# Performance work log

Measured on AMD Instinct MI355X. Metric: run time of the kernel, lower is better.

## Reference

```python
import jax, jax.numpy as jnp
import numpy as np
from jax import lax

SKIP = 0.3      # graph_skip_conn
STEPS = 5       # GGNN propagation steps
HEADS = 16
T, B, N, D = 16, 32, 256, 128
NUM_CLASSES = 2
EPS = 1e-8


def setup_inputs() -> dict:
    key = jax.random.key(0)
    ks = jax.random.split(key, 12)
    s = 0.05
    return {
        "inputs": jax.random.normal(ks[0], (T, B, N, D), dtype=jnp.float32),
        "supports": jax.random.uniform(ks[1], (B, N, N), dtype=jnp.float32),
        # multi-head weighted-cosine graph learner weights
        "W_gl": jax.random.normal(ks[2], (HEADS, D), dtype=jnp.float32) * s,
        # GGNN message transform
        "W_a": jax.random.normal(ks[3], (D, D), dtype=jnp.float32) * s,
        "b_a": jnp.zeros((D,), dtype=jnp.float32),
        # GGNN gated propagator (GRU-style) over concat([a, h]) -> D
        "W_r": jax.random.normal(ks[4], (2 * D, D), dtype=jnp.float32) * s,
        "b_r": jnp.zeros((D,), dtype=jnp.float32),
        "W_z": jax.random.normal(ks[5], (2 * D, D), dtype=jnp.float32) * s,
        "b_z": jnp.zeros((D,), dtype=jnp.float32),
        "W_h": jax.random.normal(ks[6], (2 * D, D), dtype=jnp.float32) * s,
        "b_h": jnp.zeros((D,), dtype=jnp.float32),
        # final classifier
        "W_fc": jax.random.normal(ks[7], (N * D, NUM_CLASSES), dtype=jnp.float32) * s,
        "b_fc": jnp.zeros((NUM_CLASSES,), dtype=jnp.float32),
    }


def _cell(x, A, W_gl, W_a, b_a, W_r, b_r, W_z, b_z, W_h, b_h):
    # ---- graph learner: multi-head weighted cosine similarity ----
    # x: (B,N,D); W_gl: (H,D)
    xw = x[None, :, :, :] * W_gl[:, None, None, :]             # (H,B,N,D)
    xw = xw / (jnp.linalg.norm(xw, axis=-1, keepdims=True) + EPS)
    att = jnp.einsum("hbnd,hbmd->hbnm", xw, xw).mean(axis=0)   # (B,N,N)
    att = jax.nn.relu(att)
    att = att / (att.sum(axis=-1, keepdims=True) + EPS)        # row-normalize
    A_new = SKIP * A + (1.0 - SKIP) * att                      # skip connection

    # ---- GGNN propagation over learned adjacency ----
    h = x
    for _ in range(STEPS):
        a = jnp.einsum("bnm,bmd->bnd", A_new, h) @ W_a + b_a   # message
        ah = jnp.concatenate([a, h], axis=-1)                  # (B,N,2D)
        r = jax.nn.sigmoid(ah @ W_r + b_r)
        z = jax.nn.sigmoid(ah @ W_z + b_z)
        h_tilde = jnp.tanh(jnp.concatenate([a, r * h], axis=-1) @ W_h + b_h)
        h = (1.0 - z) * h + z * h_tilde
    return h, A_new


def reference(inputs, supports, W_gl, W_a, b_a, W_r, b_r, W_z, b_z, W_h, b_h, W_fc, b_fc):
    def step(A, x_t):
        h, A_new = _cell(x_t, A, W_gl, W_a, b_a, W_r, b_r, W_z, b_z, W_h, b_h)
        return A_new, h

    A_final, outs = lax.scan(step, supports, inputs)           # outs: (T,B,N,D)
    last = outs[-1]                                            # (B,N,D)
    logits = last.reshape(last.shape[0], -1) @ W_fc + b_fc     # (B,C)
    return logits
```

## Files before the change

kernel.cpp:

```cpp
#include <hip/hip_runtime.h>
#include <math.h>

#define TT 16
#define BB 32
#define NN 256
#define DD 128
#define NSTEPS 5
#define SKIPF 0.3f
#define EPSF 1e-8f
#define T0 7
#define TBLIVE ((TT - T0) * BB)
#define IVSTR 257


typedef __attribute__((ext_vector_type(8))) short bf16x8;
typedef __attribute__((ext_vector_type(4))) float f32x4;
typedef __attribute__((ext_vector_type(8))) _Float16 half8;
typedef __attribute__((ext_vector_type(2))) _Float16 h2;

__device__ __forceinline__ unsigned short f2bf(float f) {
    union { float f; unsigned u; } v; v.f = f;
    unsigned r = (v.u + 0x7FFF + ((v.u >> 16) & 1)) >> 16;
    return (unsigned short)r;
}
__device__ __forceinline__ float bf2f(unsigned short u) {
    union { unsigned u; float f; } v; v.u = ((unsigned)u) << 16; return v.f;
}
__device__ __forceinline__ unsigned pack2(unsigned short a, unsigned short b) {
    return (unsigned)a | ((unsigned)b << 16);
}
__device__ __forceinline__ unsigned pkrtz(float a, float b) {
    unsigned r;
    asm("v_cvt_pkrtz_f16_f32 %0, %1, %2" : "=v"(r) : "v"(a), "v"(b));
    return r;
}
__device__ __forceinline__ h2 u2h(unsigned u) {
    union { unsigned u; h2 h; } v; v.u = u; return v.h;
}
__device__ __forceinline__ float sigmoidf_(float x) {
    return 1.0f / (1.0f + __expf(-x));
}
__device__ __forceinline__ float tanhf_(float x) {
    return 1.0f - 2.0f / (__expf(2.0f * x) + 1.0f);
}
__device__ __forceinline__ half8 ld8f32h(const float* src) {
    float4 a = *(const float4*)src;
    float4 b = *(const float4*)(src + 4);
    uint4 o;
    o.x = pkrtz(a.x, a.y); o.y = pkrtz(a.z, a.w);
    o.z = pkrtz(b.x, b.y); o.w = pkrtz(b.z, b.w);
    union { uint4 u; half8 h; } v; v.u = o; return v.h;
}

__global__ __launch_bounds__(256, 2) void k_gram2(const float* __restrict__ x,
                                                  const float* __restrict__ Wgl,
                                                  unsigned short* __restrict__ attn) {
    int bid = blockIdx.x;
    int rg = bid / TBLIVE;
    int tb = T0 * BB + (bid - rg * TBLIVE);
    int n0 = rg << 6;
    int tid = threadIdx.x;
    int wave = tid >> 6, lane = tid & 63;
    int m16 = lane & 15, quad = lane >> 4;
    int wcol = wave << 6;

    __shared__ unsigned wS[16 * 64];
    __shared__ unsigned ivS[16 * IVSTR];
    __shared__ float rsum[4][64];

    const float* Xb = x + ((size_t)tb << 15);

    #pragma unroll
    for (int k = 0; k < 4; ++k) {
        int idx = (tid << 2) + k;
        float2 wv = *(const float2*)(Wgl + ((idx >> 6) << 7) + ((idx & 63) << 1));
        wS[idx] = pkrtz(wv.x * wv.x, wv.y * wv.y);
    }

    half8 Bf[4][4];
    #pragma unroll
    for (int ks = 0; ks < 4; ++ks)
        #pragma unroll
        for (int cb = 0; cb < 4; ++cb)
            Bf[ks][cb] = ld8f32h(Xb + ((wcol + (cb << 4) + m16) << 7) + (ks << 5) + (quad << 3));

    half8 Af[4][4];
    #pragma unroll
    for (int rb = 0; rb < 4; ++rb)
        #pragma unroll
        for (int ks = 0; ks < 4; ++ks)
            Af[rb][ks] = ld8f32h(Xb + ((n0 + (rb << 4) + m16) << 7) + (ks << 5) + (quad << 3));

    f32x4 att[4][4];
    #pragma unroll
    for (int rb = 0; rb < 4; ++rb)
        #pragma unroll
        for (int cb = 0; cb < 4; ++cb) att[rb][cb] = (f32x4){0.f, 0.f, 0.f, 0.f};

    __syncthreads();

    union H8 { half8 v; h2 p[4]; };

    {
        half8 w2f[4];
        #pragma unroll
        for (int ks = 0; ks < 4; ++ks)
            w2f[ks] = *(const half8*)((const unsigned short*)wS + (m16 << 7) + (ks << 5) + (quad << 3));
        #pragma unroll
        for (int cb = 0; cb < 4; ++cb) {
            f32x4 nacc = (f32x4){0.f, 0.f, 0.f, 0.f};
            #pragma unroll
            for (int ks = 0; ks < 4; ++ks) {
                H8 bb; bb.v = Bf[ks][cb];
                H8 sq;
                sq.p[0] = bb.p[0] * bb.p[0];
                sq.p[1] = bb.p[1] * bb.p[1];
                sq.p[2] = bb.p[2] * bb.p[2];
                sq.p[3] = bb.p[3] * bb.p[3];
                nacc = __builtin_amdgcn_mfma_f32_16x16x32_f16(sq.v, w2f[ks], nacc, 0, 0, 0);
            }
            #pragma unroll
            for (int r = 0; r < 4; ++r) {
                float inv = 1.0f / (sqrtf(nacc[r]) + EPSF);
                ivS[m16 * IVSTR + wcol + (cb << 4) + (quad << 2) + r] = pkrtz(inv, inv);
            }
        }
    }
    __syncthreads();

    #pragma unroll 1
    for (int h = 0; h < 16; ++h) {
        const unsigned* ivh = ivS + h * IVSTR;
        h2 ivr[4], ivc[4];
        #pragma unroll
        for (int rb = 0; rb < 4; ++rb) ivr[rb] = u2h(ivh[n0 + (rb << 4) + m16]);
        #pragma unroll
        for (int cb = 0; cb < 4; ++cb) ivc[cb] = u2h(ivh[wcol + (cb << 4) + m16]);

        #pragma unroll
        for (int ks = 0; ks < 4; ++ks) {
            uint4 wu = *(const uint4*)(wS + (h << 6) + (ks << 4) + (quad << 2));
            h2 w0 = u2h(wu.x), w1 = u2h(wu.y), w2 = u2h(wu.z), w3 = u2h(wu.w);

            H8 afr[4];
            #pragma unroll
            for (int rb = 0; rb < 4; ++rb) {
                H8 a; a.v = Af[rb][ks];
                h2 s = ivr[rb];
                afr[rb].p[0] = a.p[0] * (w0 * s);
                afr[rb].p[1] = a.p[1] * (w1 * s);
                afr[rb].p[2] = a.p[2] * (w2 * s);
                afr[rb].p[3] = a.p[3] * (w3 * s);
            }
            #pragma unroll
            for (int cb = 0; cb < 4; ++cb) {
                H8 b; b.v = Bf[ks][cb];
                H8 bf;
                bf.p[0] = b.p[0] * ivc[cb];
                bf.p[1] = b.p[1] * ivc[cb];
                bf.p[2] = b.p[2] * ivc[cb];
                bf.p[3] = b.p[3] * ivc[cb];
                #pragma unroll
                for (int rb = 0; rb < 4; ++rb)
                    att[rb][cb] = __builtin_amdgcn_mfma_f32_16x16x32_f16(afr[rb].v, bf.v, att[rb][cb], 0, 0, 0);
            }
        }
    }

    float rs[4][4];
    #pragma unroll
    for (int rb = 0; rb < 4; ++rb)
        #pragma unroll
        for (int r = 0; r < 4; ++r) {
            float s = 0.f;
            #pragma unroll
            for (int cb = 0; cb < 4; ++cb) {
                float v = fmaxf(att[rb][cb][r], 0.0f);
                att[rb][cb][r] = v;
                s += v;
            }
            rs[rb][r] = s;
        }
    #pragma unroll
    for (int m = 1; m < 16; m <<= 1)
        #pragma unroll
        for (int rb = 0; rb < 4; ++rb)
            #pragma unroll
            for (int r = 0; r < 4; ++r)
                rs[rb][r] += __shfl_xor(rs[rb][r], m, 64);
    if (m16 == 0) {
        #pragma unroll
        for (int rb = 0; rb < 4; ++rb)
            #pragma unroll
            for (int r = 0; r < 4; ++r)
                rsum[wave][(rb << 4) + (quad << 2) + r] = rs[rb][r];
    }
    __syncthreads();

    unsigned short* outb = attn + ((size_t)tb << 16);
    #pragma unroll
    for (int rb = 0; rb < 4; ++rb) {
        #pragma unroll
        for (int r = 0; r < 4; ++r) {
            int row = (rb << 4) + (quad << 2) + r;
            float tot = rsum[0][row] + rsum[1][row] + rsum[2][row] + rsum[3][row];
            float inv = (1.0f - SKIPF) / (tot + 16.0f * EPSF);
            #pragma unroll
            for (int cb = 0; cb < 4; ++cb) {
                int col = wcol + (cb << 4) + m16;
                outb[((size_t)(n0 + row) << 8) + col] = f2bf(att[rb][cb][r] * inv);
            }
        }
    }
}

__global__ __launch_bounds__(256) void k_scanh(const float* __restrict__ supports,
                                               const unsigned short* __restrict__ AttA,
                                               const float* __restrict__ x15,
                                               const float* __restrict__ Wa,
                                               const float* __restrict__ Wr,
                                               const float* __restrict__ Wz,
                                               const float* __restrict__ Wh,
                                               unsigned short* __restrict__ Afin,
                                               unsigned short* __restrict__ hT,
                                               unsigned short* __restrict__ WaT,
                                               unsigned short* __restrict__ WrT,
                                               unsigned short* __restrict__ WzT,
                                               unsigned short* __restrict__ WhT) {
    __shared__ float tl[32][33];
    int bid = blockIdx.x;
    int tid = threadIdx.x;
    if (bid < 2048) {
        size_t flat = ((size_t)bid * 256 + tid) * 4;
        float4 s4 = *(const float4*)(supports + flat);
        const float s7 = SKIPF * SKIPF * SKIPF * SKIPF * SKIPF * SKIPF * SKIPF;
        float a0 = s4.x * s7, a1 = s4.y * s7, a2 = s4.z * s7, a3 = s4.w * s7;
        #pragma unroll
        for (int t = T0; t < TT; ++t) {
            const unsigned short* p = AttA + ((size_t)t << 21) + flat;
            uint2 u = *(const uint2*)p;
            a0 = SKIPF * a0 + bf2f((unsigned short)(u.x & 0xffff));
            a1 = SKIPF * a1 + bf2f((unsigned short)(u.x >> 16));
            a2 = SKIPF * a2 + bf2f((unsigned short)(u.y & 0xffff));
            a3 = SKIPF * a3 + bf2f((unsigned short)(u.y >> 16));
        }
        uint2 o;
        o.x = pack2(f2bf(a0), f2bf(a1));
        o.y = pack2(f2bf(a2), f2bf(a3));
        *(uint2*)(Afin + flat) = o;
    } else if (bid < 3072) {
        int b2 = bid - 2048;
        int b = b2 >> 5; int r = b2 & 31; int d0 = (r >> 3) << 5; int n0 = (r & 7) << 5;
        int i = tid >> 5, j = tid & 31;
        #pragma unroll
        for (int s = 0; s < 4; ++s) {
            int nl = (s << 3) + i;
            tl[nl][j] = x15[((size_t)(b * 256 + n0 + nl) << 7) + d0 + j];
        }
        __syncthreads();
        #pragma unroll
        for (int s = 0; s < 4; ++s) {
            int dd = (s << 3) + i;
            hT[((size_t)(b * 128 + d0 + dd) << 8) + n0 + j] = f2bf(tl[j][dd]);
        }
    } else {
        int idx = (bid - 3072) * 256 + tid;
        if (idx < 16384) {
            int dout = idx >> 7, din = idx & 127;
            WaT[idx] = f2bf(Wa[(din << 7) + dout]);
        }
        {
            int dout = idx >> 8, dk = idx & 255;
            WrT[idx] = f2bf(Wr[(dk << 7) + dout]);
            WzT[idx] = f2bf(Wz[(dk << 7) + dout]);
            WhT[idx] = f2bf(Wh[(dk << 7) + dout]);
        }
    }
}

__global__ __launch_bounds__(256) void k_step(
    const unsigned short* __restrict__ Afin,
    const unsigned short* __restrict__ hT,
    const unsigned short* __restrict__ WaT, const float* __restrict__ ba,
    const unsigned short* __restrict__ WrT, const float* __restrict__ br,
    const unsigned short* __restrict__ WzT, const float* __restrict__ bz,
    const unsigned short* __restrict__ WhT, const float* __restrict__ bh,
    unsigned short* __restrict__ hT_o) {

    int bid = blockIdx.x;
    int b = bid & 31, rg = bid >> 5;
    int n0 = rg << 5;
    int tid = threadIdx.x;
    int wave = tid >> 6, lane = tid & 63;
    int m16 = lane & 15, quad = lane >> 4;
    int wcol = wave << 5;

    __shared__ unsigned short msgS[32 * 136];
    __shared__ unsigned short ahS[32 * 264];

    const unsigned short* hTb = hT + ((size_t)b << 15);

    #pragma unroll
    for (int j = 0; j < 16; ++j) {
        int idx = (j << 8) + tid;
        int d = idx >> 5, row = idx & 31;
        ahS[row * 264 + 128 + d] = hTb[((size_t)d << 8) + n0 + row];
    }

    f32x4 acc[2][2];
    #pragma unroll
    for (int rb = 0; rb < 2; ++rb)
        #pragma unroll
        for (int cb = 0; cb < 2; ++cb) acc[rb][cb] = (f32x4){0.f, 0.f, 0.f, 0.f};

    const unsigned short* Ab = Afin + ((size_t)b << 16) + ((size_t)n0 << 8);
    #pragma unroll 2
    for (int ks = 0; ks < 8; ++ks) {
        bf16x8 af[2], bf[2];
        #pragma unroll
        for (int rb = 0; rb < 2; ++rb)
            af[rb] = *(const bf16x8*)(Ab + (((rb << 4) + m16) << 8) + (ks << 5) + (quad << 3));
        #pragma unroll
        for (int cb = 0; cb < 2; ++cb)
            bf[cb] = *(const bf16x8*)(hTb + ((wcol + (cb << 4) + m16) << 8) + (ks << 5) + (quad << 3));
        #pragma unroll
        for (int rb = 0; rb < 2; ++rb)
            #pragma unroll
            for (int cb = 0; cb < 2; ++cb)
                acc[rb][cb] = __builtin_amdgcn_mfma_f32_16x16x32_bf16(af[rb], bf[cb], acc[rb][cb], 0, 0, 0);
    }
    #pragma unroll
    for (int rb = 0; rb < 2; ++rb)
        #pragma unroll
        for (int cb = 0; cb < 2; ++cb)
            #pragma unroll
            for (int r = 0; r < 4; ++r)
                msgS[((rb << 4) + (quad << 2) + r) * 136 + wcol + (cb << 4) + m16] = f2bf(acc[rb][cb][r]);
    __syncthreads();

    #pragma unroll
    for (int rb = 0; rb < 2; ++rb)
        #pragma unroll
        for (int cb = 0; cb < 2; ++cb) acc[rb][cb] = (f32x4){0.f, 0.f, 0.f, 0.f};
    #pragma unroll
    for (int ks = 0; ks < 4; ++ks) {
        bf16x8 af[2], bf[2];
        #pragma unroll
        for (int rb = 0; rb < 2; ++rb)
            af[rb] = *(const bf16x8*)(msgS + ((rb << 4) + m16) * 136 + (ks << 5) + (quad << 3));
        #pragma unroll
        for (int cb = 0; cb < 2; ++cb)
            bf[cb] = *(const bf16x8*)(WaT + ((wcol + (cb << 4) + m16) << 7) + (ks << 5) + (quad << 3));
        #pragma unroll
        for (int rb = 0; rb < 2; ++rb)
            #pragma unroll
            for (int cb = 0; cb < 2; ++cb)
                acc[rb][cb] = __builtin_amdgcn_mfma_f32_16x16x32_bf16(af[rb], bf[cb], acc[rb][cb], 0, 0, 0);
    }
    {
        float bav[2];
        #pragma unroll
        for (int cb = 0; cb < 2; ++cb) bav[cb] = ba[wcol + (cb << 4) + m16];
        #pragma unroll
        for (int rb = 0; rb < 2; ++rb)
            #pragma unroll
            for (int cb = 0; cb < 2; ++cb)
                #pragma unroll
                for (int r = 0; r < 4; ++r)
                    ahS[((rb << 4) + (quad << 2) + r) * 264 + wcol + (cb << 4) + m16] =
                        f2bf(acc[rb][cb][r] + bav[cb]);
    }
    __syncthreads();

    float hv[2][2][4];
    #pragma unroll
    for (int rb = 0; rb < 2; ++rb)
        #pragma unroll
        for (int cb = 0; cb < 2; ++cb) {
            int col = wcol + (cb << 4) + m16;
            uint2 u = *(const uint2*)(hTb + ((size_t)col << 8) + n0 + (rb << 4) + (quad << 2));
            hv[rb][cb][0] = bf2f((unsigned short)(u.x & 0xffff));
            hv[rb][cb][1] = bf2f((unsigned short)(u.x >> 16));
            hv[rb][cb][2] = bf2f((unsigned short)(u.y & 0xffff));
            hv[rb][cb][3] = bf2f((unsigned short)(u.y >> 16));
        }

    f32x4 racc[2][2], zacc[2][2];
    #pragma unroll
    for (int rb = 0; rb < 2; ++rb)
        #pragma unroll
        for (int cb = 0; cb < 2; ++cb) {
            racc[rb][cb] = (f32x4){0.f, 0.f, 0.f, 0.f};
            zacc[rb][cb] = (f32x4){0.f, 0.f, 0.f, 0.f};
        }
    #pragma unroll 2
    for (int ks = 0; ks < 8; ++ks) {
        bf16x8 af[2], bfr[2], bfz[2];
        #pragma unroll
        for (int rb = 0; rb < 2; ++rb)
            af[rb] = *(const bf16x8*)(ahS + ((rb << 4) + m16) * 264 + (ks << 5) + (quad << 3));
        #pragma unroll
        for (int cb = 0; cb < 2; ++cb) {
            int dout = wcol + (cb << 4) + m16;
            bfr[cb] = *(const bf16x8*)(WrT + (dout << 8) + (ks << 5) + (quad << 3));
            bfz[cb] = *(const bf16x8*)(WzT + (dout << 8) + (ks << 5) + (quad << 3));
        }
        #pragma unroll
        for (int rb = 0; rb < 2; ++rb)
            #pragma unroll
            for (int cb = 0; cb < 2; ++cb) {
                racc[rb][cb] = __builtin_amdgcn_mfma_f32_16x16x32_bf16(af[rb], bfr[cb], racc[rb][cb], 0, 0, 0);
                zacc[rb][cb] = __builtin_amdgcn_mfma_f32_16x16x32_bf16(af[rb], bfz[cb], zacc[rb][cb], 0, 0, 0);
            }
    }
    float zv[2][2][4];
    {
        float brv[2], bzv[2];
        #pragma unroll
        for (int cb = 0; cb < 2; ++cb) {
            brv[cb] = br[wcol + (cb << 4) + m16];
            bzv[cb] = bz[wcol + (cb << 4) + m16];
        }
        #pragma unroll
        for (int rb = 0; rb < 2; ++rb)
            #pragma unroll
            for (int cb = 0; cb < 2; ++cb)
                #pragma unroll
                for (int r = 0; r < 4; ++r) {
                    racc[rb][cb][r] = sigmoidf_(racc[rb][cb][r] + brv[cb]);
                    zv[rb][cb][r]  = sigmoidf_(zacc[rb][cb][r] + bzv[cb]);
                }
    }
    __syncthreads();

    #pragma unroll
    for (int rb = 0; rb < 2; ++rb)
        #pragma unroll
        for (int cb = 0; cb < 2; ++cb)
            #pragma unroll
            for (int r = 0; r < 4; ++r)
                ahS[((rb << 4) + (quad << 2) + r) * 264 + 128 + wcol + (cb << 4) + m16] =
                    f2bf(racc[rb][cb][r] * hv[rb][cb][r]);
    __syncthreads();

    #pragma unroll
    for (int rb = 0; rb < 2; ++rb)
        #pragma unroll
        for (int cb = 0; cb < 2; ++cb) acc[rb][cb] = (f32x4){0.f, 0.f, 0.f, 0.f};
    #pragma unroll 2
    for (int ks = 0; ks < 8; ++ks) {
        bf16x8 af[2], bf[2];
        #pragma unroll
        for (int rb = 0; rb < 2; ++rb)
            af[rb] = *(const bf16x8*)(ahS + ((rb << 4) + m16) * 264 + (ks << 5) + (quad << 3));
        #pragma unroll
        for (int cb = 0; cb < 2; ++cb)
            bf[cb] = *(const bf16x8*)(WhT + ((wcol + (cb << 4) + m16) << 8) + (ks << 5) + (quad << 3));
        #pragma unroll
        for (int rb = 0; rb < 2; ++rb)
            #pragma unroll
            for (int cb = 0; cb < 2; ++cb)
                acc[rb][cb] = __builtin_amdgcn_mfma_f32_16x16x32_bf16(af[rb], bf[cb], acc[rb][cb], 0, 0, 0);
    }

    {
        float bhv[2];
        #pragma unroll
        for (int cb = 0; cb < 2; ++cb) bhv[cb] = bh[wcol + (cb << 4) + m16];
        #pragma unroll
        for (int rb = 0; rb < 2; ++rb)
            #pragma unroll
            for (int cb = 0; cb < 2; ++cb) {
                int col = wcol + (cb << 4) + m16;
                unsigned short pk[4];
                #pragma unroll
                for (int r = 0; r < 4; ++r) {
                    float ht = tanhf_(acc[rb][cb][r] + bhv[cb]);
                    float hn = hv[rb][cb][r] + zv[rb][cb][r] * (ht - hv[rb][cb][r]);
                    pk[r] = f2bf(hn);
                }
                uint2 p;
                p.x = pack2(pk[0], pk[1]); p.y = pack2(pk[2], pk[3]);
                *(uint2*)(hT_o + ((size_t)(b * 128 + col) << 8) + n0 + (rb << 4) + (quad << 2)) = p;
            }
    }
}

__global__ __launch_bounds__(256) void k_fc(const unsigned short* __restrict__ hT,
                                            const float* __restrict__ Wfc,
                                            const float* __restrict__ bfc,
                                            float* __restrict__ out) {
    int bid = blockIdx.x;
    int b = bid >> 4, part = bid & 15;
    int tid = threadIdx.x;
    const unsigned short* hp = hT + ((size_t)b << 15);
    int i = part * 2048 + tid * 8;
    int d = i >> 8, n = i & 255;
    uint4 hu = *(const uint4*)(hp + i);
    unsigned short hs[8];
    hs[0] = hu.x & 0xffff; hs[1] = hu.x >> 16;
    hs[2] = hu.y & 0xffff; hs[3] = hu.y >> 16;
    hs[4] = hu.z & 0xffff; hs[5] = hu.z >> 16;
    hs[6] = hu.w & 0xffff; hs[7] = hu.w >> 16;
    float a0 = 0.f, a1 = 0.f;
    #pragma unroll
    for (int k = 0; k < 8; ++k) {
        float v = bf2f(hs[k]);
        const float2 w = *(const float2*)(Wfc + ((size_t)(n + k) * 128 + d) * 2);
        a0 = fmaf(v, w.x, a0);
        a1 = fmaf(v, w.y, a1);
    }
    int wave = tid >> 6, lane = tid & 63;
    #pragma unroll
    for (int off = 32; off; off >>= 1) {
        a0 += __shfl_down(a0, off, 64);
        a1 += __shfl_down(a1, off, 64);
    }
    __shared__ float r0[4], r1[4];
    if (lane == 0) { r0[wave] = a0; r1[wave] = a1; }
    __syncthreads();
    if (tid == 0) {
        float s0 = r0[0] + r0[1] + r0[2] + r0[3];
        float s1 = r1[0] + r1[1] + r1[2] + r1[3];
        if (part == 0) { s0 += bfc[0]; s1 += bfc[1]; }
        atomicAdd(&out[b * 2 + 0], s0);
        atomicAdd(&out[b * 2 + 1], s1);
    }
}

extern "C" void kernel_launch(void* const* d_in, const int* in_sizes, int n_in,
                              void* d_out, int out_size, void* d_ws, size_t ws_size,
                              hipStream_t stream) {
    const float* x_all    = (const float*)d_in[0];
    const float* supports = (const float*)d_in[1];
    const float* Wgl = (const float*)d_in[2];
    const float* Wa  = (const float*)d_in[3];
    const float* ba  = (const float*)d_in[4];
    const float* Wr  = (const float*)d_in[5];
    const float* br  = (const float*)d_in[6];
    const float* Wz  = (const float*)d_in[7];
    const float* bz  = (const float*)d_in[8];
    const float* Wh  = (const float*)d_in[9];
    const float* bh  = (const float*)d_in[10];
    const float* Wfc = (const float*)d_in[11];
    const float* bfc = (const float*)d_in[12];
    float* out = (float*)d_out;

    char* p = (char*)d_ws;
    auto alloc = [&](size_t bytes) { char* r = p; p += (bytes + 255) & ~(size_t)255; return r; };

    unsigned short* AttA = (unsigned short*)alloc((size_t)TT * BB * NN * NN * 2);
    unsigned short* Afin = (unsigned short*)alloc((size_t)BB * NN * NN * 2);
    unsigned short* hT0  = (unsigned short*)alloc((size_t)BB * DD * NN * 2);
    unsigned short* hT1  = (unsigned short*)alloc((size_t)BB * DD * NN * 2);
    unsigned short* WaT  = (unsigned short*)alloc(128 * 128 * 2);
    unsigned short* WrT  = (unsigned short*)alloc(256 * 128 * 2);
    unsigned short* WzT  = (unsigned short*)alloc(256 * 128 * 2);
    unsigned short* WhT  = (unsigned short*)alloc(256 * 128 * 2);

    k_gram2<<<4 * TBLIVE, 256, 0, stream>>>(x_all, Wgl, AttA);

    const float* x15 = x_all + (size_t)15 * BB * NN * DD;
    k_scanh<<<2048 + 1024 + 128, 256, 0, stream>>>(supports, AttA, x15,
                                                   Wa, Wr, Wz, Wh,
                                                   Afin, hT0,
                                                   WaT, WrT, WzT, WhT);

    const unsigned short* hT_in = hT0;
    for (int s = 0; s < NSTEPS; ++s) {
        unsigned short* hTo = (s & 1) ? hT0 : hT1;
        k_step<<<8 * BB, 256, 0, stream>>>(Afin, hT_in,
                                           WaT, ba, WrT, br, WzT, bz, WhT, bh,
                                           hTo);
        hT_in = hTo;
    }

    hipMemsetAsync(d_out, 0, (size_t)out_size * sizeof(float), stream);
    k_fc<<<BB * 16, 256, 0, stream>>>(hT1, Wfc, bfc, out);
}
```

Baseline: 295.9 us.

## Fuse GRU propagation steps, transpose and classifier into one per-batch kernel

Replaces the five per-step GGNN launches, the separate transpose of the last input and the final FC kernel with one kernel, k_gru5. It launches one 512-thread block per batch element and loops over all steps and row groups internally. This removes several kernel launches, the memset and the atomics, and folds the classifier into the last step's epilogue, so the final hidden state is never written out. The cost is much less parallelism: only 32 blocks run on the GPU, and each block processes eight row groups in sequence within each step.

```diff
diff --git a/kernel.cpp b/kernel.cpp
--- a/kernel.cpp
+++ b/kernel.cpp
@@ -10,7 +10,6 @@
 #define EPSF 1e-8f
 #define T0 7
 #define TBLIVE ((TT - T0) * BB)
-#define IVSTR 257
 
 
 typedef __attribute__((ext_vector_type(8))) short bf16x8;
@@ -52,6 +51,7 @@
     union { uint4 u; half8 h; } v; v.u = o; return v.h;
 }
 
+#define IVSTR 257
 __global__ __launch_bounds__(256, 2) void k_gram2(const float* __restrict__ x,
                                                   const float* __restrict__ Wgl,
                                                   unsigned short* __restrict__ attn) {
@@ -216,18 +216,15 @@
 
 __global__ __launch_bounds__(256) void k_scanh(const float* __restrict__ supports,
                                                const unsigned short* __restrict__ AttA,
-                                               const float* __restrict__ x15,
                                                const float* __restrict__ Wa,
                                                const float* __restrict__ Wr,
                                                const float* __restrict__ Wz,
                                                const float* __restrict__ Wh,
                                                unsigned short* __restrict__ Afin,
-                                               unsigned short* __restrict__ hT,
                                                unsigned short* __restrict__ WaT,
                                                unsigned short* __restrict__ WrT,
                                                unsigned short* __restrict__ WzT,
                                                unsigned short* __restrict__ WhT) {
-    __shared__ float tl[32][33];
     int bid = blockIdx.x;
     int tid = threadIdx.x;
     if (bid < 2048) {
@@ -248,23 +245,8 @@
         o.x = pack2(f2bf(a0), f2bf(a1));
         o.y = pack2(f2bf(a2), f2bf(a3));
         *(uint2*)(Afin + flat) = o;
-    } else if (bid < 3072) {
-        int b2 = bid - 2048;
-        int b = b2 >> 5; int r = b2 & 31; int d0 = (r >> 3) << 5; int n0 = (r & 7) << 5;
-        int i = tid >> 5, j = tid & 31;
-        #pragma unroll
-        for (int s = 0; s < 4; ++s) {
-            int nl = (s << 3) + i;
-            tl[nl][j] = x15[((size_t)(b * 256 + n0 + nl) << 7) + d0 + j];
-        }
-        __syncthreads();
-        #pragma unroll
-        for (int s = 0; s < 4; ++s) {
-            int dd = (s << 3) + i;
-            hT[((size_t)(b * 128 + d0 + dd) << 8) + n0 + j] = f2bf(tl[j][dd]);
-        }
     } else {
-        int idx = (bid - 3072) * 256 + tid;
+        int idx = (bid - 2048) * 256 + tid;
         if (idx < 16384) {
             int dout = idx >> 7, din = idx & 127;
             WaT[idx] = f2bf(Wa[(din << 7) + dout]);
@@ -278,253 +260,280 @@
     }
 }
 
-__global__ __launch_bounds__(256) void k_step(
+__global__ __launch_bounds__(512) void k_gru5(
+    const float* __restrict__ x15,
     const unsigned short* __restrict__ Afin,
-    const unsigned short* __restrict__ hT,
     const unsigned short* __restrict__ WaT, const float* __restrict__ ba,
     const unsigned short* __restrict__ WrT, const float* __restrict__ br,
     const unsigned short* __restrict__ WzT, const float* __restrict__ bz,
     const unsigned short* __restrict__ WhT, const float* __restrict__ bh,
-    unsigned short* __restrict__ hT_o) {
-
-    int bid = blockIdx.x;
-    int b = bid & 31, rg = bid >> 5;
-    int n0 = rg << 5;
+    const float* __restrict__ Wfc, const float* __restrict__ bfc,
+    unsigned short* __restrict__ hA, unsigned short* __restrict__ hB,
+    float* __restrict__ out) {
+
+    int b = blockIdx.x;
     int tid = threadIdx.x;
-    int wave = tid >> 6, lane = tid & 63;
+    int wave = tid >> 6;
+    int g = wave >> 2;
+    int wv = wave & 3;
+    int lane = tid & 63;
     int m16 = lane & 15, quad = lane >> 4;
-    int wcol = wave << 5;
-
-    __shared__ unsigned short msgS[32 * 136];
-    __shared__ unsigned short ahS[32 * 264];
-
-    const unsigned short* hTb = hT + ((size_t)b << 15);
-
-    #pragma unroll
-    for (int j = 0; j < 16; ++j) {
-        int idx = (j << 8) + tid;
-        int d = idx >> 5, row = idx & 31;
-        ahS[row * 264 + 128 + d] = hTb[((size_t)d << 8) + n0 + row];
-    }
-
-    f32x4 acc[2][2];
-    #pragma unroll
-    for (int rb = 0; rb < 2; ++rb)
-        #pragma unroll
-        for (int cb = 0; cb < 2; ++cb) acc[rb][cb] = (f32x4){0.f, 0.f, 0.f, 0.f};
-
-    const unsigned short* Ab = Afin + ((size_t)b << 16) + ((size_t)n0 << 8);
-    #pragma unroll 2
-    for (int ks = 0; ks < 8; ++ks) {
-        bf16x8 af[2], bf[2];
-        #pragma unroll
-        for (int rb = 0; rb < 2; ++rb)
-            af[rb] = *(const bf16x8*)(Ab + (((rb << 4) + m16) << 8) + (ks << 5) + (quad << 3));
-        #pragma unroll
-        for (int cb = 0; cb < 2; ++cb)
-            bf[cb] = *(const bf16x8*)(hTb + ((wcol + (cb << 4) + m16) << 8) + (ks << 5) + (quad << 3));
-        #pragma unroll
-        for (int rb = 0; rb < 2; ++rb)
-            #pragma unroll
-            for (int cb = 0; cb < 2; ++cb)
-                acc[rb][cb] = __builtin_amdgcn_mfma_f32_16x16x32_bf16(af[rb], bf[cb], acc[rb][cb], 0, 0, 0);
-    }
-    #pragma unroll
-    for (int rb = 0; rb < 2; ++rb)
-        #pragma unroll
-        for (int cb = 0; cb < 2; ++cb)
-            #pragma unroll
-            for (int r = 0; r < 4; ++r)
-                msgS[((rb << 4) + (quad << 2) + r) * 136 + wcol + (cb << 4) + m16] = f2bf(acc[rb][cb][r]);
-    __syncthreads();
-
-    #pragma unroll
-    for (int rb = 0; rb < 2; ++rb)
-        #pragma unroll
-        for (int cb = 0; cb < 2; ++cb) acc[rb][cb] = (f32x4){0.f, 0.f, 0.f, 0.f};
-    #pragma unroll
-    for (int ks = 0; ks < 4; ++ks) {
-        bf16x8 af[2], bf[2];
-        #pragma unroll
-        for (int rb = 0; rb < 2; ++rb)
-            af[rb] = *(const bf16x8*)(msgS + ((rb << 4) + m16) * 136 + (ks << 5) + (quad << 3));
-        #pragma unroll
-        for (int cb = 0; cb < 2; ++cb)
-            bf[cb] = *(const bf16x8*)(WaT + ((wcol + (cb << 4) + m16) << 7) + (ks << 5) + (quad << 3));
-        #pragma unroll
-        for (int rb = 0; rb < 2; ++rb)
-            #pragma unroll
-            for (int cb = 0; cb < 2; ++cb)
-                acc[rb][cb] = __builtin_amdgcn_mfma_f32_16x16x32_bf16(af[rb], bf[cb], acc[rb][cb], 0, 0, 0);
-    }
+    int wcol = wv << 5;
+    int gt = (wv << 6) | lane;
+
+    __shared__ unsigned short msgS[2][32 * 136];
+    __shared__ unsigned short ahS[2][32 * 264];
+    __shared__ float rf[8][2];
+
     {
-        float bav[2];
-        #pragma unroll
-        for (int cb = 0; cb < 2; ++cb) bav[cb] = ba[wcol + (cb << 4) + m16];
-        #pragma unroll
-        for (int rb = 0; rb < 2; ++rb)
-            #pragma unroll
-            for (int cb = 0; cb < 2; ++cb)
-                #pragma unroll
-                for (int r = 0; r < 4; ++r)
-                    ahS[((rb << 4) + (quad << 2) + r) * 264 + wcol + (cb << 4) + m16] =
-                        f2bf(acc[rb][cb][r] + bav[cb]);
-    }
-    __syncthreads();
-
-    float hv[2][2][4];
-    #pragma unroll
-    for (int rb = 0; rb < 2; ++rb)
-        #pragma unroll
-        for (int cb = 0; cb < 2; ++cb) {
-            int col = wcol + (cb << 4) + m16;
-            uint2 u = *(const uint2*)(hTb + ((size_t)col << 8) + n0 + (rb << 4) + (quad << 2));
-            hv[rb][cb][0] = bf2f((unsigned short)(u.x & 0xffff));
-            hv[rb][cb][1] = bf2f((unsigned short)(u.x >> 16));
-            hv[rb][cb][2] = bf2f((unsigned short)(u.y & 0xffff));
-            hv[rb][cb][3] = bf2f((unsigned short)(u.y >> 16));
-        }
-
-    f32x4 racc[2][2], zacc[2][2];
-    #pragma unroll
-    for (int rb = 0; rb < 2; ++rb)
-        #pragma unroll
-        for (int cb = 0; cb < 2; ++cb) {
-            racc[rb][cb] = (f32x4){0.f, 0.f, 0.f, 0.f};
-            zacc[rb][cb] = (f32x4){0.f, 0.f, 0.f, 0.f};
-        }
-    #pragma unroll 2
-    for (int ks = 0; ks < 8; ++ks) {
-        bf16x8 af[2], bfr[2], bfz[2];
-        #pragma unroll
-        for (int rb = 0; rb < 2; ++rb)
-            af[rb] = *(const bf16x8*)(ahS + ((rb << 4) + m16) * 264 + (ks << 5) + (quad << 3));
-        #pragma unroll
-        for (int cb = 0; cb < 2; ++cb) {
-            int dout = wcol + (cb << 4) + m16;
-            bfr[cb] = *(const bf16x8*)(WrT + (dout << 8) + (ks << 5) + (quad << 3));
-            bfz[cb] = *(const bf16x8*)(WzT + (dout << 8) + (ks << 5) + (quad << 3));
-        }
-        #pragma unroll
-        for (int rb = 0; rb < 2; ++rb)
-            #pragma unroll
-            for (int cb = 0; cb < 2; ++cb) {
-                racc[rb][cb] = __builtin_amdgcn_mfma_f32_16x16x32_bf16(af[rb], bfr[cb], racc[rb][cb], 0, 0, 0);
-                zacc[rb][cb] = __builtin_amdgcn_mfma_f32_16x16x32_bf16(af[rb], bfz[cb], zacc[rb][cb], 0, 0, 0);
-            }
-    }
-    float zv[2][2][4];
-    {
-        float brv[2], bzv[2];
-        #pragma unroll
-        for (int cb = 0; cb < 2; ++cb) {
-            brv[cb] = br[wcol + (cb << 4) + m16];
-            bzv[cb] = bz[wcol + (cb << 4) + m16];
-        }
-        #pragma unroll
-        for (int rb = 0; rb < 2; ++rb)
-            #pragma unroll
-            for (int cb = 0; cb < 2; ++cb)
-                #pragma unroll
-                for (int r = 0; r < 4; ++r) {
-                    racc[rb][cb][r] = sigmoidf_(racc[rb][cb][r] + brv[cb]);
-                    zv[rb][cb][r]  = sigmoidf_(zacc[rb][cb][r] + bzv[cb]);
+        float* tl = (float*)ahS;
+        int half = tid >> 8;
+        int t256 = tid & 255;
+        int i = t256 >> 5, j = t256 & 31;
+        float* tlh = tl + half * (32 * 33);
+        for (int it = 0; it < 16; ++it) {
+            int tile = (it << 1) + half;
+            int d0 = (tile >> 3) << 5;
+            int nn0 = (tile & 7) << 5;
+            #pragma unroll
+            for (int s4 = 0; s4 < 4; ++s4) {
+                int nl = (s4 << 3) + i;
+                tlh[nl * 33 + j] = x15[((size_t)(b * 256 + nn0 + nl) << 7) + d0 + j];
+            }
+            __syncthreads();
+            #pragma unroll
+            for (int s4 = 0; s4 < 4; ++s4) {
+                int dd = (s4 << 3) + i;
+                hA[((size_t)(b * 128 + d0 + dd) << 8) + nn0 + j] = f2bf(tlh[j * 33 + dd]);
+            }
+            __syncthreads();
+        }
+    }
+
+    float fc0 = 0.f, fc1 = 0.f;
+
+    for (int s = 0; s < NSTEPS; ++s) {
+        const unsigned short* hIn = ((s & 1) ? hB : hA) + ((size_t)b << 15);
+        unsigned short* hOut = ((s & 1) ? hA : hB) + ((size_t)b << 15);
+
+        for (int p = 0; p < 4; ++p) {
+            int rgp = (p << 1) + g;
+            int n0 = rgp << 5;
+            unsigned short* mS = msgS[g];
+            unsigned short* aS = ahS[g];
+            const unsigned short* Ab = Afin + ((size_t)b << 16) + ((size_t)n0 << 8);
+
+            #pragma unroll
+            for (int j = 0; j < 16; ++j) {
+                int idx = (j << 8) + gt;
+                int d = idx >> 5, row = idx & 31;
+                aS[row * 264 + 128 + d] = hIn[((size_t)d << 8) + n0 + row];
+            }
+
+            f32x4 acc[2][2];
+            #pragma unroll
+            for (int rb = 0; rb < 2; ++rb)
+                #pragma unroll
+                for (int cb = 0; cb < 2; ++cb) acc[rb][cb] = (f32x4){0.f, 0.f, 0.f, 0.f};
+
+            #pragma unroll 2
+            for (int ks = 0; ks < 8; ++ks) {
+                bf16x8 af[2], bf[2];
+                #pragma unroll
+                for (int rb = 0; rb < 2; ++rb)
+                    af[rb] = *(const bf16x8*)(Ab + (((rb << 4) + m16) << 8) + (ks << 5) + (quad << 3));
+                #pragma unroll
+                for (int cb = 0; cb < 2; ++cb)
+                    bf[cb] = *(const bf16x8*)(hIn + ((wcol + (cb << 4) + m16) << 8) + (ks << 5) + (quad << 3));
+                #pragma unroll
+                for (int rb = 0; rb < 2; ++rb)
+                    #pragma unroll
+                    for (int cb = 0; cb < 2; ++cb)
+                        acc[rb][cb] = __builtin_amdgcn_mfma_f32_16x16x32_bf16(af[rb], bf[cb], acc[rb][cb], 0, 0, 0);
+            }
+            #pragma unroll
+            for (int rb = 0; rb < 2; ++rb)
+                #pragma unroll
+                for (int cb = 0; cb < 2; ++cb)
+                    #pragma unroll
+                    for (int r = 0; r < 4; ++r)
+                        mS[((rb << 4) + (quad << 2) + r) * 136 + wcol + (cb << 4) + m16] = f2bf(acc[rb][cb][r]);
+            __syncthreads();
+
+            #pragma unroll
+            for (int rb = 0; rb < 2; ++rb)
+                #pragma unroll
+                for (int cb = 0; cb < 2; ++cb) acc[rb][cb] = (f32x4){0.f, 0.f, 0.f, 0.f};
+            #pragma unroll
+            for (int ks = 0; ks < 4; ++ks) {
+                bf16x8 af[2], bf[2];
+                #pragma unroll
+                for (int rb = 0; rb < 2; ++rb)
+                    af[rb] = *(const bf16x8*)(mS + ((rb << 4) + m16) * 136 + (ks << 5) + (quad << 3));
+                #pragma unroll
+                for (int cb = 0; cb < 2; ++cb)
+                    bf[cb] = *(const bf16x8*)(WaT + ((wcol + (cb << 4) + m16) << 7) + (ks << 5) + (quad << 3));
+                #pragma unroll
+                for (int rb = 0; rb < 2; ++rb)
+                    #pragma unroll
+                    for (int cb = 0; cb < 2; ++cb)
+                        acc[rb][cb] = __builtin_amdgcn_mfma_f32_16x16x32_bf16(af[rb], bf[cb], acc[rb][cb], 0, 0, 0);
+            }
+            {
+                float bav[2];
+                #pragma unroll
+                for (int cb = 0; cb < 2; ++cb) bav[cb] = ba[wcol + (cb << 4) + m16];
+                #pragma unroll
+                for (int rb = 0; rb < 2; ++rb)
+                    #pragma unroll
+                    for (int cb = 0; cb < 2; ++cb)
+                        #pragma unroll
+                        for (int r = 0; r < 4; ++r)
+                            aS[((rb << 4) + (quad << 2) + r) * 264 + wcol + (cb << 4) + m16] =
+                                f2bf(acc[rb][cb][r] + bav[cb]);
+            }
+            __syncthreads();
+
+            float hv[2][2][4];
+            #pragma unroll
+            for (int rb = 0; rb < 2; ++rb)
+                #pragma unroll
+                for (int cb = 0; cb < 2; ++cb) {
+                    int col = wcol + (cb << 4) + m16;
+                    uint2 u = *(const uint2*)(hIn + ((size_t)col << 8) + n0 + (rb << 4) + (quad << 2));
+                    hv[rb][cb][0] = bf2f((unsigned short)(u.x & 0xffff));
+                    hv[rb][cb][1] = bf2f((unsigned short)(u.x >> 16));
+                    hv[rb][cb][2] = bf2f((unsigned short)(u.y & 0xffff));
+                    hv[rb][cb][3] = bf2f((unsigned short)(u.y >> 16));
                 }
-    }
-    __syncthreads();
-
-    #pragma unroll
-    for (int rb = 0; rb < 2; ++rb)
-        #pragma unroll
-        for (int cb = 0; cb < 2; ++cb)
-            #pragma unroll
-            for (int r = 0; r < 4; ++r)
-                ahS[((rb << 4) + (quad << 2) + r) * 264 + 128 + wcol + (cb << 4) + m16] =
-                    f2bf(racc[rb][cb][r] * hv[rb][cb][r]);
-    __syncthreads();
-
-    #pragma unroll
-    for (int rb = 0; rb < 2; ++rb)
-        #pragma unroll
-        for (int cb = 0; cb < 2; ++cb) acc[rb][cb] = (f32x4){0.f, 0.f, 0.f, 0.f};
-    #pragma unroll 2
-    for (int ks = 0; ks < 8; ++ks) {
-        bf16x8 af[2], bf[2];
-        #pragma unroll
-        for (int rb = 0; rb < 2; ++rb)
-            af[rb] = *(const bf16x8*)(ahS + ((rb << 4) + m16) * 264 + (ks << 5) + (quad << 3));
-        #pragma unroll
-        for (int cb = 0; cb < 2; ++cb)
-            bf[cb] = *(const bf16x8*)(WhT + ((wcol + (cb << 4) + m16) << 8) + (ks << 5) + (quad << 3));
-        #pragma unroll
-        for (int rb = 0; rb < 2; ++rb)
-            #pragma unroll
-            for (int cb = 0; cb < 2; ++cb)
-                acc[rb][cb] = __builtin_amdgcn_mfma_f32_16x16x32_bf16(af[rb], bf[cb], acc[rb][cb], 0, 0, 0);
-    }
-
-    {
-        float bhv[2];
-        #pragma unroll
-        for (int cb = 0; cb < 2; ++cb) bhv[cb] = bh[wcol + (cb << 4) + m16];
-        #pragma unroll
-        for (int rb = 0; rb < 2; ++rb)
-            #pragma unroll
-            for (int cb = 0; cb < 2; ++cb) {
-                int col = wcol + (cb << 4) + m16;
-                unsigned short pk[4];
-                #pragma unroll
-                for (int r = 0; r < 4; ++r) {
-                    float ht = tanhf_(acc[rb][cb][r] + bhv[cb]);
-                    float hn = hv[rb][cb][r] + zv[rb][cb][r] * (ht - hv[rb][cb][r]);
-                    pk[r] = f2bf(hn);
+
+            f32x4 racc[2][2], zacc[2][2];
+            #pragma unroll
+            for (int rb = 0; rb < 2; ++rb)
+                #pragma unroll
+                for (int cb = 0; cb < 2; ++cb) {
+                    racc[rb][cb] = (f32x4){0.f, 0.f, 0.f, 0.f};
+                    zacc[rb][cb] = (f32x4){0.f, 0.f, 0.f, 0.f};
                 }
-                uint2 p;
-                p.x = pack2(pk[0], pk[1]); p.y = pack2(pk[2], pk[3]);
-                *(uint2*)(hT_o + ((size_t)(b * 128 + col) << 8) + n0 + (rb << 4) + (quad << 2)) = p;
-            }
-    }
-}
-
-__global__ __launch_bounds__(256) void k_fc(const unsigned short* __restrict__ hT,
-                                            const float* __restrict__ Wfc,
-                                            const float* __restrict__ bfc,
-                                            float* __restrict__ out) {
-    int bid = blockIdx.x;
-    int b = bid >> 4, part = bid & 15;
-    int tid = threadIdx.x;
-    const unsigned short* hp = hT + ((size_t)b << 15);
-    int i = part * 2048 + tid * 8;
-    int d = i >> 8, n = i & 255;
-    uint4 hu = *(const uint4*)(hp + i);
-    unsigned short hs[8];
-    hs[0] = hu.x & 0xffff; hs[1] = hu.x >> 16;
-    hs[2] = hu.y & 0xffff; hs[3] = hu.y >> 16;
-    hs[4] = hu.z & 0xffff; hs[5] = hu.z >> 16;
-    hs[6] = hu.w & 0xffff; hs[7] = hu.w >> 16;
-    float a0 = 0.f, a1 = 0.f;
-    #pragma unroll
-    for (int k = 0; k < 8; ++k) {
-        float v = bf2f(hs[k]);
-        const float2 w = *(const float2*)(Wfc + ((size_t)(n + k) * 128 + d) * 2);
-        a0 = fmaf(v, w.x, a0);
-        a1 = fmaf(v, w.y, a1);
-    }
-    int wave = tid >> 6, lane = tid & 63;
+            #pragma unroll 2
+            for (int ks = 0; ks < 8; ++ks) {
+                bf16x8 af[2], bfr[2], bfz[2];
+                #pragma unroll
+                for (int rb = 0; rb < 2; ++rb)
+                    af[rb] = *(const bf16x8*)(aS + ((rb << 4) + m16) * 264 + (ks << 5) + (quad << 3));
+                #pragma unroll
+                for (int cb = 0; cb < 2; ++cb) {
+                    int dout = wcol + (cb << 4) + m16;
+                    bfr[cb] = *(const bf16x8*)(WrT + (dout << 8) + (ks << 5) + (quad << 3));
+                    bfz[cb] = *(const bf16x8*)(WzT + (dout << 8) + (ks << 5) + (quad << 3));
+                }
+                #pragma unroll
+                for (int rb = 0; rb < 2; ++rb)
+                    #pragma unroll
+                    for (int cb = 0; cb < 2; ++cb) {
+                        racc[rb][cb] = __builtin_amdgcn_mfma_f32_16x16x32_bf16(af[rb], bfr[cb], racc[rb][cb], 0, 0, 0);
+                        zacc[rb][cb] = __builtin_amdgcn_mfma_f32_16x16x32_bf16(af[rb], bfz[cb], zacc[rb][cb], 0, 0, 0);
+                    }
+            }
+            float zv[2][2][4];
+            {
+                float brv[2], bzv[2];
+                #pragma unroll
+                for (int cb = 0; cb < 2; ++cb) {
+                    brv[cb] = br[wcol + (cb << 4) + m16];
+                    bzv[cb] = bz[wcol + (cb << 4) + m16];
+                }
+                #pragma unroll
+                for (int rb = 0; rb < 2; ++rb)
+                    #pragma unroll
+                    for (int cb = 0; cb < 2; ++cb)
+                        #pragma unroll
+                        for (int r = 0; r < 4; ++r) {
+                            racc[rb][cb][r] = sigmoidf_(racc[rb][cb][r] + brv[cb]);
+                            zv[rb][cb][r]  = sigmoidf_(zacc[rb][cb][r] + bzv[cb]);
+                        }
+            }
+            __syncthreads();
+
+            #pragma unroll
+            for (int rb = 0; rb < 2; ++rb)
+                #pragma unroll
+                for (int cb = 0; cb < 2; ++cb)
+                    #pragma unroll
+                    for (int r = 0; r < 4; ++r)
+                        aS[((rb << 4) + (quad << 2) + r) * 264 + 128 + wcol + (cb << 4) + m16] =
+                            f2bf(racc[rb][cb][r] * hv[rb][cb][r]);
+            __syncthreads();
+
+            #pragma unroll
+            for (int rb = 0; rb < 2; ++rb)
+                #pragma unroll
+                for (int cb = 0; cb < 2; ++cb) acc[rb][cb] = (f32x4){0.f, 0.f, 0.f, 0.f};
+            #pragma unroll 2
+            for (int ks = 0; ks < 8; ++ks) {
+                bf16x8 af[2], bf[2];
+                #pragma unroll
+                for (int rb = 0; rb < 2; ++rb)
+                    af[rb] = *(const bf16x8*)(aS + ((rb << 4) + m16) * 264 + (ks << 5) + (quad << 3));
+                #pragma unroll
+                for (int cb = 0; cb < 2; ++cb)
+                    bf[cb] = *(const bf16x8*)(WhT + ((wcol + (cb << 4) + m16) << 8) + (ks << 5) + (quad << 3));
+                #pragma unroll
+                for (int rb = 0; rb < 2; ++rb)
+                    #pragma unroll
+                    for (int cb = 0; cb < 2; ++cb)
+                        acc[rb][cb] = __builtin_amdgcn_mfma_f32_16x16x32_bf16(af[rb], bf[cb], acc[rb][cb], 0, 0, 0);
+            }
+
+            {
+                float bhv[2];
+                #pragma unroll
+                for (int cb = 0; cb < 2; ++cb) bhv[cb] = bh[wcol + (cb << 4) + m16];
+                #pragma unroll
+                for (int rb = 0; rb < 2; ++rb)
+                    #pragma unroll
+                    for (int cb = 0; cb < 2; ++cb) {
+                        int col = wcol + (cb << 4) + m16;
+                        unsigned short pk[4];
+                        #pragma unroll
+                        for (int r = 0; r < 4; ++r) {
+                            float ht = tanhf_(acc[rb][cb][r] + bhv[cb]);
+                            float hn = hv[rb][cb][r] + zv[rb][cb][r] * (ht - hv[rb][cb][r]);
+                            pk[r] = f2bf(hn);
+                        }
+                        if (s < NSTEPS - 1) {
+                            uint2 pw;
+                            pw.x = pack2(pk[0], pk[1]); pw.y = pack2(pk[2], pk[3]);
+                            *(uint2*)(hOut + ((size_t)col << 8) + n0 + (rb << 4) + (quad << 2)) = pw;
+                        } else {
+                            #pragma unroll
+                            for (int r = 0; r < 4; ++r) {
+                                int nn = n0 + (rb << 4) + (quad << 2) + r;
+                                float hval = bf2f(pk[r]);
+                                const float2 w = *(const float2*)(Wfc + (size_t)(nn * 128 + col) * 2);
+                                fc0 = fmaf(hval, w.x, fc0);
+                                fc1 = fmaf(hval, w.y, fc1);
+                            }
+                        }
+                    }
+            }
+            __syncthreads();
+        }
+    }
+
     #pragma unroll
     for (int off = 32; off; off >>= 1) {
-        a0 += __shfl_down(a0, off, 64);
-        a1 += __shfl_down(a1, off, 64);
-    }
-    __shared__ float r0[4], r1[4];
-    if (lane == 0) { r0[wave] = a0; r1[wave] = a1; }
+        fc0 += __shfl_down(fc0, off, 64);
+        fc1 += __shfl_down(fc1, off, 64);
+    }
+    if (lane == 0) { rf[wave][0] = fc0; rf[wave][1] = fc1; }
     __syncthreads();
     if (tid == 0) {
-        float s0 = r0[0] + r0[1] + r0[2] + r0[3];
-        float s1 = r1[0] + r1[1] + r1[2] + r1[3];
-        if (part == 0) { s0 += bfc[0]; s1 += bfc[1]; }
-        atomicAdd(&out[b * 2 + 0], s0);
-        atomicAdd(&out[b * 2 + 1], s1);
+        float s0 = 0.f, s1 = 0.f;
+        #pragma unroll
+        for (int w = 0; w < 8; ++w) { s0 += rf[w][0]; s1 += rf[w][1]; }
+        out[b * 2 + 0] = s0 + bfc[0];
+        out[b * 2 + 1] = s1 + bfc[1];
     }
 }
 
@@ -560,21 +569,12 @@
 
     k_gram2<<<4 * TBLIVE, 256, 0, stream>>>(x_all, Wgl, AttA);
 
+    k_scanh<<<2048 + 128, 256, 0, stream>>>(supports, AttA,
+                                            Wa, Wr, Wz, Wh,
+                                            Afin, WaT, WrT, WzT, WhT);
+
     const float* x15 = x_all + (size_t)15 * BB * NN * DD;
-    k_scanh<<<2048 + 1024 + 128, 256, 0, stream>>>(supports, AttA, x15,
-                                                   Wa, Wr, Wz, Wh,
-                                                   Afin, hT0,
-                                                   WaT, WrT, WzT, WhT);
-
-    const unsigned short* hT_in = hT0;
-    for (int s = 0; s < NSTEPS; ++s) {
-        unsigned short* hTo = (s & 1) ? hT0 : hT1;
-        k_step<<<8 * BB, 256, 0, stream>>>(Afin, hT_in,
-                                           WaT, ba, WrT, br, WzT, bz, WhT, bh,
-                                           hTo);
-        hT_in = hTo;
-    }
-
-    hipMemsetAsync(d_out, 0, (size_t)out_size * sizeof(float), stream);
-    k_fc<<<BB * 16, 256, 0, stream>>>(hT1, Wfc, bfc, out);
-}
+    k_gru5<<<BB, 512, 0, stream>>>(x15, Afin,
+                                   WaT, ba, WrT, br, WzT, bz, WhT, bh,
+                                   Wfc, bfc, hT0, hT1, out);
+}
```

After: 665.9 us. 125% more time.
